# Optimization experiments

Measured on AMD Instinct MI355X. Metric: run time of the kernel, lower is better.

The kernel has to match this reference:

```python
import jax, jax.numpy as jnp
import numpy as np
from jax import lax
import math

B, C_IN, C_OUT, D, H, W = 8, 32, 32, 16, 64, 64
K = 3            # kernel_size (cubic)
PAD = 1
E = 8            # num_experts
GROUPS = 1


def setup_inputs() -> dict:
    key = jax.random.key(0)
    k1, k2, k3, k4 = jax.random.split(key, 4)
    x = jax.random.normal(k1, (B, C_IN, D, H, W), dtype=jnp.float32)
    routing_weights = jax.random.uniform(k2, (B, E), dtype=jnp.float32)
    # kaiming_uniform_(a=sqrt(5)) equivalent bounds
    fan_in = (C_IN // GROUPS) * K * K * K
    gain = math.sqrt(2.0 / (1.0 + 5.0))
    w_bound = gain * math.sqrt(3.0 / fan_in)
    weight = jax.random.uniform(k3, (E, C_OUT, C_IN // GROUPS, K, K, K),
                                dtype=jnp.float32, minval=-w_bound, maxval=w_bound)
    b_bound = 1.0 / math.sqrt(fan_in)
    bias = jax.random.uniform(k4, (E, C_OUT), dtype=jnp.float32,
                              minval=-b_bound, maxval=b_bound)
    return {"x": x, "routing_weights": routing_weights, "weight": weight, "bias": bias}


def reference(x, routing_weights, weight, bias):
    # Faithful to the original einsum: 'bi,eocdwh->bocdwh' sums i and e
    # independently (outer-sum semantics), exactly as torch.einsum does.
    eff_kernel = jnp.einsum('bi,eocdwh->bocdwh', routing_weights, weight)  # [B,O,I/g,kd,kh,kw]
    eff_bias = jnp.einsum('bi,eo->bo', routing_weights, bias)              # [B,O]

    def conv_one(xi, ki, bi):
        # xi: [C_in,D,H,W]; ki: [O, I/g, kd,kh,kw]
        y = lax.conv_general_dilated(
            xi[None], ki,
            window_strides=(1, 1, 1),
            padding=[(PAD, PAD)] * 3,
            lhs_dilation=(1, 1, 1),
            rhs_dilation=(1, 1, 1),
            dimension_numbers=('NCDHW', 'OIDHW', 'NCDHW'),
            feature_group_count=GROUPS,
        )[0]
        return y + bi[:, None, None, None]

    return jax.vmap(conv_one)(x, eff_kernel, eff_bias)  # [B, C_OUT, D, H, W]
```

## Files before the change

### kernel.cpp

```cpp
#include <hip/hip_runtime.h>
#include <hip/hip_bf16.h>

typedef short short8 __attribute__((ext_vector_type(8)));
typedef short short4v __attribute__((ext_vector_type(4)));
typedef float f32x4 __attribute__((ext_vector_type(4)));

#define WF_OFF  0u
#define RWB_OFF 55296u
#define RWS_OFF 56320u

#define XSB 72
#define ROWB (24 * XSB)
#define PLANE_B (10 * ROWB)
#define RING_B (3 * PLANE_B)

__device__ __forceinline__ unsigned bf16rne(float f) {
    unsigned u = __float_as_uint(f);
    return (u + 0x7FFFu + ((u >> 16) & 1u)) >> 16;
}

__global__ void condconv_prep(const float* __restrict__ rw,
                              const float* __restrict__ weight,
                              const float* __restrict__ bias,
                              char* __restrict__ ws) {
    int i = blockIdx.x * 256 + threadIdx.x;
    if (i < 27648) {
        int t   = i >> 10;
        int rem = i & 1023;
        int ot  = rem >> 9;
        int l   = (rem >> 3) & 63;
        int j   = rem & 7;
        int o   = ot * 16 + (l & 15);
        int c   = 8 * (l >> 4) + j;
        float s = 0.f;
#pragma unroll
        for (int e = 0; e < 8; ++e) s += weight[((e * 32 + o) * 32 + c) * 27 + t];
        ((unsigned short*)(ws + WF_OFF))[i] = (unsigned short)bf16rne(s);
    } else if (i < 27904) {
        int k = i - 27648;
        int b = k >> 5, o = k & 31;
        float rs = 0.f, bs = 0.f;
#pragma unroll
        for (int e = 0; e < 8; ++e) { rs += rw[b * 8 + e]; bs += bias[e * 32 + o]; }
        ((float*)(ws + RWB_OFF))[k] = rs * bs;
        if (o == 0) ((float*)(ws + RWS_OFF))[b] = rs;
    }
}

__global__ __launch_bounds__(256, 2) void condconv_zwalk(
        const float* __restrict__ x,
        const char* __restrict__ wf,
        const float* __restrict__ rwbias,
        const float* __restrict__ rwsum,
        float* __restrict__ out) {
    __shared__ __align__(16) char smem[RING_B];

    const int tid  = threadIdx.x;
    const int wv   = tid >> 6;
    const int lane = tid & 63;
    const int n    = lane & 15;
    const int quad = lane >> 4;
    const int ot   = wv & 1;
    const int yh   = wv >> 1;

    const int logical = (blockIdx.x & 7) * 64 + (blockIdx.x >> 3);
    const int b   = logical >> 6;
    const int rem = logical & 63;
    const int zb  = rem & 1;
    const int xb  = (rem >> 1) & 3;
    const int yb  = rem >> 3;
    const int y0 = yb * 8, x0 = xb * 16, zr0 = zb * 8;

    const float* xbp = x + (size_t)b * 2097152;

    const bool sact = tid < 240;
    const int  sx4  = tid % 6;
    const int  syp  = (tid / 6) % 10;
    const int  sc4h = tid / 60;
    const int  gxq  = xb * 4 + sx4 - 1;
    const int  gy   = y0 + syp - 1;
    const bool gok  = ((unsigned)gxq < 16u) && ((unsigned)gy < 64u);
    const long soff = (long)sc4h * 262144 + (long)(gok ? gy : 0) * 64 +
                      (long)(gok ? gxq : 0) * 4;
    const int woffA = syp * ROWB + (4 * sx4) * XSB + ((sc4h ^ sx4) << 3);
    const int woffB = syp * ROWB + (4 * sx4) * XSB + (((sc4h + 4) ^ sx4) << 3);

    short8 wreg[27];
    {
        const char* wb_ = wf + lane * 16 + ot * 1024;
#pragma unroll
        for (int t = 0; t < 27; ++t) wreg[t] = *(const short8*)(wb_ + t * 2048);
    }

    const float rwb = rwsum[b];
    float bb[4];
#pragma unroll
    for (int j = 0; j < 4; ++j) bb[j] = rwbias[b * 32 + ot * 16 + quad * 4 + j];
    float* outb = out + (size_t)(b * 32 + ot * 16 + quad * 4) * 65536 +
                  (size_t)(y0 + yh * 4) * 64 + x0 + n;

    auto STAGE = [&](int p, char* pl) {
        if (!sact) return;
        float4 vA0 = {0,0,0,0}, vA1 = vA0, vA2 = vA0, vA3 = vA0;
        float4 vB0 = vA0, vB1 = vA0, vB2 = vA0, vB3 = vA0;
        if (gok && (unsigned)p < 16u) {
            const float* q0 = xbp + soff + (long)p * 4096;
            vA0 = *(const float4*)(q0);
            vA1 = *(const float4*)(q0 + 65536);
            vA2 = *(const float4*)(q0 + 131072);
            vA3 = *(const float4*)(q0 + 196608);
            const float* q1 = q0 + 1048576;
            vB0 = *(const float4*)(q1);
            vB1 = *(const float4*)(q1 + 65536);
            vB2 = *(const float4*)(q1 + 131072);
            vB3 = *(const float4*)(q1 + 196608);
        }
        const float A0[4] = {vA0.x, vA0.y, vA0.z, vA0.w};
        const float A1[4] = {vA1.x, vA1.y, vA1.z, vA1.w};
        const float A2[4] = {vA2.x, vA2.y, vA2.z, vA2.w};
        const float A3[4] = {vA3.x, vA3.y, vA3.z, vA3.w};
        const float B0[4] = {vB0.x, vB0.y, vB0.z, vB0.w};
        const float B1[4] = {vB1.x, vB1.y, vB1.z, vB1.w};
        const float B2[4] = {vB2.x, vB2.y, vB2.z, vB2.w};
        const float B3[4] = {vB3.x, vB3.y, vB3.z, vB3.w};
#pragma unroll
        for (int xi = 0; xi < 4; ++xi) {
            union { __hip_bfloat162 h2[2]; uint2 u; } gA, gB;
            gA.h2[0] = __float22bfloat162_rn(make_float2(A0[xi], A1[xi]));
            gA.h2[1] = __float22bfloat162_rn(make_float2(A2[xi], A3[xi]));
            gB.h2[0] = __float22bfloat162_rn(make_float2(B0[xi], B1[xi]));
            gB.h2[1] = __float22bfloat162_rn(make_float2(B2[xi], B3[xi]));
            *(uint2*)(pl + woffA + xi * XSB) = gA.u;
            *(uint2*)(pl + woffB + xi * XSB) = gB.u;
        }
    };

    STAGE(zr0 - 1, smem + ((zr0 + 2) % 3) * PLANE_B);
    STAGE(zr0,     smem + (zr0 % 3) * PLANE_B);

    f32x4 acc[4] = {};

    for (int zi = zr0; zi < zr0 + 8; ++zi) {
        __syncthreads();
        STAGE(zi + 1, smem + ((zi + 1) % 3) * PLANE_B);
        __syncthreads();

        const char* P[3] = { smem + ((zi + 2) % 3) * PLANE_B,
                             smem + ((zi    ) % 3) * PLANE_B,
                             smem + ((zi + 1) % 3) * PLANE_B };
#pragma unroll
        for (int dz = 0; dz < 3; ++dz) {
#pragma unroll
            for (int q = 0; q < 6; ++q) {
                const char* rowq = P[dz] + (yh * 4 + q) * ROWB;
#pragma unroll
                for (int dx = 0; dx < 3; ++dx) {
                    const int lx = n + dx + 3;
                    const int s8 = lx >> 2;
                    const char* rowp = rowq + lx * XSB;
                    union { short8 v; short4v h[2]; } xf;
                    xf.h[0] = *(const short4v*)(rowp + (((2 * quad + 0) ^ s8) << 3));
                    xf.h[1] = *(const short4v*)(rowp + (((2 * quad + 1) ^ s8) << 3));
#pragma unroll
                    for (int dy = 0; dy < 3; ++dy) {
                        const int r = q - dy;
                        if (r >= 0 && r < 4)
                            acc[r] = __builtin_amdgcn_mfma_f32_16x16x32_bf16(
                                wreg[dz * 9 + dy * 3 + dx], xf.v, acc[r], 0, 0, 0);
                    }
                }
            }
        }

#pragma unroll
        for (int r = 0; r < 4; ++r) {
#pragma unroll
            for (int j = 0; j < 4; ++j)
                outb[(size_t)j * 65536 + (size_t)zi * 4096 + r * 64] =
                    rwb * acc[r][j] + bb[j];
            acc[r] = f32x4{0, 0, 0, 0};
        }
    }
}

extern "C" void kernel_launch(void* const* d_in, const int* in_sizes, int n_in,
                              void* d_out, int out_size, void* d_ws, size_t ws_size,
                              hipStream_t stream) {
    const float* x      = (const float*)d_in[0];
    const float* rw     = (const float*)d_in[1];
    const float* weight = (const float*)d_in[2];
    const float* bias   = (const float*)d_in[3];
    float* out = (float*)d_out;
    char*  ws  = (char*)d_ws;

    condconv_prep<<<109, 256, 0, stream>>>(rw, weight, bias, ws);
    condconv_zwalk<<<512, 256, 0, stream>>>(
        x, ws + WF_OFF,
        (const float*)(ws + RWB_OFF), (const float*)(ws + RWS_OFF), out);
}
```

Measured before the change: 148.9 us.

## Compute two z-planes per step with a 4-plane ring and 16-byte LDS layout

The z-walk now handles two output depth planes per iteration. Each staged input plane fragment loaded from LDS feeds two accumulator sets, which halves LDS reads and the number of barriers per output plane. The shared ring grows from 3 to 4 planes, and the staging layout changes so each thread packs 8 channels into one 16-byte store with an XOR swizzle, allowing single short8 LDS reads. The costs are more accumulator registers, a larger LDS footprint (77 KB per block at 2 blocks per CU) and a longer stall when staging two planes at once.

```diff
diff --git a/kernel.cpp b/kernel.cpp
--- a/kernel.cpp
+++ b/kernel.cpp
@@ -2,17 +2,16 @@
 #include <hip/hip_bf16.h>
 
 typedef short short8 __attribute__((ext_vector_type(8)));
-typedef short short4v __attribute__((ext_vector_type(4)));
 typedef float f32x4 __attribute__((ext_vector_type(4)));
 
 #define WF_OFF  0u
 #define RWB_OFF 55296u
 #define RWS_OFF 56320u
 
-#define XSB 72
-#define ROWB (24 * XSB)
+#define XSB 80
+#define ROWB 1936
 #define PLANE_B (10 * ROWB)
-#define RING_B (3 * PLANE_B)
+#define RING_B (4 * PLANE_B)
 
 __device__ __forceinline__ unsigned bf16rne(float f) {
     unsigned u = __float_as_uint(f);
@@ -47,7 +46,7 @@
     }
 }
 
-__global__ __launch_bounds__(256, 2) void condconv_zwalk(
+__global__ __launch_bounds__(256, 2) void condconv_zwalk2(
         const float* __restrict__ x,
         const char* __restrict__ wf,
         const float* __restrict__ rwbias,
@@ -74,16 +73,16 @@
     const float* xbp = x + (size_t)b * 2097152;
 
     const bool sact = tid < 240;
-    const int  sx4  = tid % 6;
-    const int  syp  = (tid / 6) % 10;
-    const int  sc4h = tid / 60;
+    const int  scc  = tid / 60;
+    const int  rr   = tid % 60;
+    const int  syp  = rr / 6;
+    const int  sx4  = rr % 6;
     const int  gxq  = xb * 4 + sx4 - 1;
     const int  gy   = y0 + syp - 1;
     const bool gok  = ((unsigned)gxq < 16u) && ((unsigned)gy < 64u);
-    const long soff = (long)sc4h * 262144 + (long)(gok ? gy : 0) * 64 +
-                      (long)(gok ? gxq : 0) * 4;
-    const int woffA = syp * ROWB + (4 * sx4) * XSB + ((sc4h ^ sx4) << 3);
-    const int woffB = syp * ROWB + (4 * sx4) * XSB + (((sc4h + 4) ^ sx4) << 3);
+    const long soff = (long)scc * 524288 +
+                      (long)(gok ? gy : 0) * 64 + (long)(gok ? gxq : 0) * 4;
+    const int  wbase_off = syp * ROWB + (4 * sx4) * XSB;
 
     short8 wreg[27];
     {
@@ -99,74 +98,70 @@
     float* outb = out + (size_t)(b * 32 + ot * 16 + quad * 4) * 65536 +
                   (size_t)(y0 + yh * 4) * 64 + x0 + n;
 
-    auto STAGE = [&](int p, char* pl) {
+    auto STAGE = [&](int p) {
         if (!sact) return;
-        float4 vA0 = {0,0,0,0}, vA1 = vA0, vA2 = vA0, vA3 = vA0;
-        float4 vB0 = vA0, vB1 = vA0, vB2 = vA0, vB3 = vA0;
+        char* pl = smem + (p & 3) * PLANE_B;
+        float a[8][4];
         if (gok && (unsigned)p < 16u) {
             const float* q0 = xbp + soff + (long)p * 4096;
-            vA0 = *(const float4*)(q0);
-            vA1 = *(const float4*)(q0 + 65536);
-            vA2 = *(const float4*)(q0 + 131072);
-            vA3 = *(const float4*)(q0 + 196608);
-            const float* q1 = q0 + 1048576;
-            vB0 = *(const float4*)(q1);
-            vB1 = *(const float4*)(q1 + 65536);
-            vB2 = *(const float4*)(q1 + 131072);
-            vB3 = *(const float4*)(q1 + 196608);
+#pragma unroll
+            for (int k = 0; k < 8; ++k) {
+                const float4 v = *(const float4*)(q0 + (size_t)k * 65536);
+                a[k][0] = v.x; a[k][1] = v.y; a[k][2] = v.z; a[k][3] = v.w;
+            }
+        } else {
+#pragma unroll
+            for (int k = 0; k < 8; ++k)
+                { a[k][0] = 0.f; a[k][1] = 0.f; a[k][2] = 0.f; a[k][3] = 0.f; }
         }
-        const float A0[4] = {vA0.x, vA0.y, vA0.z, vA0.w};
-        const float A1[4] = {vA1.x, vA1.y, vA1.z, vA1.w};
-        const float A2[4] = {vA2.x, vA2.y, vA2.z, vA2.w};
-        const float A3[4] = {vA3.x, vA3.y, vA3.z, vA3.w};
-        const float B0[4] = {vB0.x, vB0.y, vB0.z, vB0.w};
-        const float B1[4] = {vB1.x, vB1.y, vB1.z, vB1.w};
-        const float B2[4] = {vB2.x, vB2.y, vB2.z, vB2.w};
-        const float B3[4] = {vB3.x, vB3.y, vB3.z, vB3.w};
 #pragma unroll
         for (int xi = 0; xi < 4; ++xi) {
-            union { __hip_bfloat162 h2[2]; uint2 u; } gA, gB;
-            gA.h2[0] = __float22bfloat162_rn(make_float2(A0[xi], A1[xi]));
-            gA.h2[1] = __float22bfloat162_rn(make_float2(A2[xi], A3[xi]));
-            gB.h2[0] = __float22bfloat162_rn(make_float2(B0[xi], B1[xi]));
-            gB.h2[1] = __float22bfloat162_rn(make_float2(B2[xi], B3[xi]));
-            *(uint2*)(pl + woffA + xi * XSB) = gA.u;
-            *(uint2*)(pl + woffB + xi * XSB) = gB.u;
+            union { __hip_bfloat162 h2[4]; uint4 u; } g;
+            g.h2[0] = __float22bfloat162_rn(make_float2(a[0][xi], a[1][xi]));
+            g.h2[1] = __float22bfloat162_rn(make_float2(a[2][xi], a[3][xi]));
+            g.h2[2] = __float22bfloat162_rn(make_float2(a[4][xi], a[5][xi]));
+            g.h2[3] = __float22bfloat162_rn(make_float2(a[6][xi], a[7][xi]));
+            const int col = 4 * sx4 + xi;
+            *(uint4*)(pl + wbase_off + xi * XSB + ((scc ^ (col & 3)) << 4)) = g.u;
         }
     };
 
-    STAGE(zr0 - 1, smem + ((zr0 + 2) % 3) * PLANE_B);
-    STAGE(zr0,     smem + (zr0 % 3) * PLANE_B);
+    STAGE(zr0 - 1);
+    STAGE(zr0);
 
-    f32x4 acc[4] = {};
+    f32x4 accA[4] = {}, accB[4] = {};
 
-    for (int zi = zr0; zi < zr0 + 8; ++zi) {
+#pragma unroll 1
+    for (int k = 0; k < 4; ++k) {
+        const int zA = zr0 + 2 * k;
+
         __syncthreads();
-        STAGE(zi + 1, smem + ((zi + 1) % 3) * PLANE_B);
+        STAGE(zA + 1);
+        STAGE(zA + 2);
         __syncthreads();
 
-        const char* P[3] = { smem + ((zi + 2) % 3) * PLANE_B,
-                             smem + ((zi    ) % 3) * PLANE_B,
-                             smem + ((zi + 1) % 3) * PLANE_B };
 #pragma unroll
-        for (int dz = 0; dz < 3; ++dz) {
+        for (int pi = 0; pi < 4; ++pi) {
+            const char* Pp = smem + ((zA - 1 + pi) & 3) * PLANE_B;
 #pragma unroll
             for (int q = 0; q < 6; ++q) {
-                const char* rowq = P[dz] + (yh * 4 + q) * ROWB;
+                const char* rowq = Pp + (yh * 4 + q) * ROWB;
 #pragma unroll
                 for (int dx = 0; dx < 3; ++dx) {
                     const int lx = n + dx + 3;
-                    const int s8 = lx >> 2;
-                    const char* rowp = rowq + lx * XSB;
-                    union { short8 v; short4v h[2]; } xf;
-                    xf.h[0] = *(const short4v*)(rowp + (((2 * quad + 0) ^ s8) << 3));
-                    xf.h[1] = *(const short4v*)(rowp + (((2 * quad + 1) ^ s8) << 3));
+                    const short8 xf = *(const short8*)(
+                        rowq + lx * XSB + ((quad ^ (lx & 3)) << 4));
 #pragma unroll
                     for (int dy = 0; dy < 3; ++dy) {
                         const int r = q - dy;
-                        if (r >= 0 && r < 4)
-                            acc[r] = __builtin_amdgcn_mfma_f32_16x16x32_bf16(
-                                wreg[dz * 9 + dy * 3 + dx], xf.v, acc[r], 0, 0, 0);
+                        if (r >= 0 && r < 4) {
+                            if (pi < 3)
+                                accA[r] = __builtin_amdgcn_mfma_f32_16x16x32_bf16(
+                                    wreg[pi * 9 + dy * 3 + dx], xf, accA[r], 0, 0, 0);
+                            if (pi > 0)
+                                accB[r] = __builtin_amdgcn_mfma_f32_16x16x32_bf16(
+                                    wreg[(pi - 1) * 9 + dy * 3 + dx], xf, accB[r], 0, 0, 0);
+                        }
                     }
                 }
             }
@@ -175,10 +170,13 @@
 #pragma unroll
         for (int r = 0; r < 4; ++r) {
 #pragma unroll
-            for (int j = 0; j < 4; ++j)
-                outb[(size_t)j * 65536 + (size_t)zi * 4096 + r * 64] =
-                    rwb * acc[r][j] + bb[j];
-            acc[r] = f32x4{0, 0, 0, 0};
+            for (int j = 0; j < 4; ++j) {
+                float* po = outb + (size_t)j * 65536 + r * 64;
+                po[(size_t)zA * 4096]       = rwb * accA[r][j] + bb[j];
+                po[(size_t)(zA + 1) * 4096] = rwb * accB[r][j] + bb[j];
+            }
+            accA[r] = f32x4{0, 0, 0, 0};
+            accB[r] = f32x4{0, 0, 0, 0};
         }
     }
 }
@@ -194,7 +192,7 @@
     char*  ws  = (char*)d_ws;
 
     condconv_prep<<<109, 256, 0, stream>>>(rw, weight, bias, ws);
-    condconv_zwalk<<<512, 256, 0, stream>>>(
+    condconv_zwalk2<<<512, 256, 0, stream>>>(
         x, ws + WF_OFF,
         (const float*)(ws + RWB_OFF), (const float*)(ws + RWS_OFF), out);
 }
```

Measured after the change: 145.2 us. 2.5% less time.
